# Kernel tuning notes

Measured on AMD Instinct MI355X. Metric: run time of the kernel, lower is better.

The kernel has to match this reference:

```python
import jax, jax.numpy as jnp
import numpy as np

N, C, R, G, K = 4096, 128, 128, 6, 16
RADIUS = 0.8
C_OUT = 64
FLAT = G * G * G * C_OUT  # 13824


def setup_inputs() -> dict:
    key = jax.random.key(0)
    ks = jax.random.split(key, 24)
    xav = lambda k, shp: (jax.random.normal(k, shp, jnp.float32)
                          * np.sqrt(2.0 / (shp[0] + shp[1])).astype(np.float32))
    # scene points in ~[-5,5]^3 so radius-0.8 balls hold ~8 points on average
    xyz = jax.random.normal(ks[0], (N, 3), jnp.float32) * 2.5
    feats = jax.random.normal(ks[1], (N, C), jnp.float32)
    ctr = jax.random.normal(ks[2], (R, 3), jnp.float32) * 2.5
    size = jax.random.uniform(ks[3], (R, 3), jnp.float32) * 3.0 + 1.0
    yaw = jax.random.uniform(ks[4], (R, 1), jnp.float32) * (2.0 * np.pi)
    rois = jnp.concatenate([ctr, size, yaw], -1)  # [R,7] (x,y,z,dx,dy,dz,ry)
    return {
        'xyz': xyz, 'feats': feats, 'rois': rois,
        'w_m1': xav(ks[5], (3 + C, C_OUT)), 'w_m2': xav(ks[6], (C_OUT, C_OUT)),
        'w_s1': xav(ks[7], (FLAT, 1024)), 'w_s2': xav(ks[8], (1024, 512)),
        'w_c1': xav(ks[9], (512, 1024)), 'w_c2': xav(ks[10], (1024, 512)),
        'w_c3': xav(ks[11], (512, 1)), 'b_c3': jnp.zeros((1,), jnp.float32),
        'w_i1': xav(ks[12], (512, 1024)), 'w_i2': xav(ks[13], (1024, 512)),
        'w_i3': xav(ks[14], (512, 1)), 'b_i3': jnp.zeros((1,), jnp.float32),
        'w_r1': xav(ks[15], (512, 1024)), 'w_r2': xav(ks[16], (1024, 512)),
        'w_r3': jax.random.normal(ks[17], (512, 7), jnp.float32) * 0.001,
        'b_r3': jnp.zeros((7,), jnp.float32),
    }


def _grid_points(rois):
    """get_dense_grid_points + rotate_points_along_z + center shift."""
    i = jnp.arange(G)
    gi, gj, gk = jnp.meshgrid(i, i, i, indexing='ij')
    dense = jnp.stack([gi, gj, gk], -1).reshape(-1, 3).astype(rois.dtype)  # [G^3,3]
    size = rois[:, 3:6]
    local = (dense[None] + 0.5) / G * size[:, None] - size[:, None] * 0.5  # [R,G^3,3]
    c, s = jnp.cos(rois[:, 6])[:, None], jnp.sin(rois[:, 6])[:, None]
    x, y, z = local[..., 0], local[..., 1], local[..., 2]
    rot = jnp.stack([x * c - y * s, x * s + y * c, z], -1)
    return rot + rois[:, None, 0:3]  # [R,G^3,3]


def reference(xyz, feats, rois, w_m1, w_m2, w_s1, w_s2,
              w_c1, w_c2, w_c3, b_c3, w_i1, w_i2, w_i3, b_i3,
              w_r1, w_r2, w_r3, b_r3):
    gp = _grid_points(rois).reshape(-1, 3)  # [M,3], M = R*G^3
    M = gp.shape[0]
    # ball query: first K point indices within RADIUS of each grid point
    d2 = jnp.sum((gp[:, None, :] - xyz[None, :, :]) ** 2, -1)  # [M,N]
    cand = jnp.where(d2 < RADIUS * RADIUS, jnp.arange(N), N)  # invalid -> N
    neg_top, _ = jax.lax.top_k(-cand, K)
    idx = -neg_top  # K smallest candidate indices, ascending-ish
    valid = idx < N
    first = idx[:, :1]
    idx = jnp.where(valid, idx, first)  # pad with first hit (pointnet2 semantics)
    empty = ~valid[:, 0]  # balls with zero neighbors
    idx = jnp.where(empty[:, None], 0, idx)
    # group: relative xyz + point features
    rel = xyz[idx] - gp[:, None, :]               # [M,K,3]
    g = jnp.concatenate([rel, feats[idx]], -1)    # [M,K,3+C]
    # shared per-point MLP (Conv2d 1x1 + identity-init BN + ReLU)
    h = jax.nn.relu(g @ w_m1)
    h = jax.nn.relu(h @ w_m2)                     # [M,K,C_OUT]
    pooled = jnp.max(h, axis=1)                   # max_pool over neighbors
    pooled = jnp.where(empty[:, None], 0.0, pooled)
    flat = pooled.reshape(rois.shape[0], -1)      # [R, G^3*C_OUT]
    # shared FC (Conv1d k=1 stacks) then cls / iou / reg heads
    sfc = jax.nn.relu(jax.nn.relu(flat @ w_s1) @ w_s2)
    head = lambda x, w1, w2, w3, b3: jax.nn.relu(jax.nn.relu(x @ w1) @ w2) @ w3 + b3
    cls = head(sfc, w_c1, w_c2, w_c3, b_c3)   # [R,1]
    iou = head(sfc, w_i1, w_i2, w_i3, b_i3)   # [R,1]
    reg = head(sfc, w_r1, w_r2, w_r3, b_r3)   # [R,7]
    return jnp.concatenate([cls, iou, reg], -1)  # [R,9]
```

## Files before the change

kernel.cpp:

```cpp
#include <hip/hip_runtime.h>

typedef float  f32x4  __attribute__((ext_vector_type(4)));
typedef __bf16 bf16x8 __attribute__((ext_vector_type(8)));
typedef unsigned short ushort_t;

#define N_PTS 4096
#define R_ROIS 128
#define M_GP  27648
#define LDS_FENCE() asm volatile("s_waitcnt lgkmcnt(0)" ::: "memory")

static constexpr size_t OFF_GP     = 0;
static constexpr size_t OFF_PH     = 331776;
static constexpr size_t OFF_PL     = 3870720;
static constexpr size_t OFF_H1H    = 331776;
static constexpr size_t OFF_H1L    = 1118208;
static constexpr size_t OFF_H2S    = 1904640;
static constexpr size_t OFF_PART   = 7409664;
static constexpr size_t OFF_CAND   = OFF_PART;
static constexpr size_t OFF_F      = 9506816;
static constexpr size_t OFF_XYZ4   = 10555392;
static constexpr size_t OFF_NCAND  = 11603968;
static constexpr size_t OFF_W1TH   = 11604480;
static constexpr size_t OFF_W1TL   = 11625984;
static constexpr size_t OFF_W2TH   = 11647488;
static constexpr size_t OFF_W2TL   = 11656704;
static constexpr size_t OFF_FHI    = 11665920;
static constexpr size_t OFF_FLO    = 12714496;
static constexpr size_t OFF_IDX    = 11665920;
static constexpr size_t OFF_T1H    = 11665920;
static constexpr size_t OFF_T1L    = 11928064;
static constexpr size_t OFF_SFCH   = 12190208;
static constexpr size_t OFF_SFCL   = 12321280;

static __device__ inline ushort_t f2bf(float f) {
    unsigned int u = __float_as_uint(f);
    unsigned int r = u + 0x7FFFu + ((u >> 16) & 1u);
    return (ushort_t)(r >> 16);
}
static __device__ inline float bf2f(ushort_t h) {
    return __uint_as_float(((unsigned int)h) << 16);
}
static __device__ inline ushort_t bfbits(__bf16 h) {
    return __builtin_bit_cast(ushort_t, h);
}

__global__ __launch_bounds__(256) void prep_all_k(
    const float* __restrict__ rois, const float* __restrict__ xyz,
    const float* __restrict__ feats, const float* __restrict__ w1,
    const float* __restrict__ w2, float* __restrict__ gp,
    ushort_t* __restrict__ fhi, ushort_t* __restrict__ flo,
    ushort_t* __restrict__ w1th, ushort_t* __restrict__ w1tl,
    ushort_t* __restrict__ w2th, ushort_t* __restrict__ w2tl,
    float4* __restrict__ xyz4,
    int* __restrict__ cand, int* __restrict__ ncand) {
    int b = blockIdx.x, tid = threadIdx.x;
    if (b < 108) {
        int m = b * 256 + tid;
        int r = m / 216, t = m % 216;
        int gi = t / 36, gj = (t / 6) % 6, gk = t % 6;
        const float* roi = rois + r * 7;
        float sx = roi[3], sy = roi[4], sz = roi[5];
        float lx = ((float)gi + 0.5f) / 6.0f * sx - sx * 0.5f;
        float ly = ((float)gj + 0.5f) / 6.0f * sy - sy * 0.5f;
        float lz = ((float)gk + 0.5f) / 6.0f * sz - sz * 0.5f;
        float c = cosf(roi[6]), s = sinf(roi[6]);
        gp[m * 3 + 0] = lx * c - ly * s + roi[0];
        gp[m * 3 + 1] = lx * s + ly * c + roi[1];
        gp[m * 3 + 2] = lz + roi[2];
    } else if (b < 150) {
        int t = (b - 108) * 256 + tid;
        {
            int col = t / 168, p = t % 168;
            float v = (p < 128) ? w1[(3 + p) * 64 + col]
                    : (p < 131) ? w1[(p - 128) * 64 + col] : 0.f;
            ushort_t hi = f2bf(v);
            w1th[t] = hi;
            w1tl[t] = f2bf(v - bf2f(hi));
        }
        if (t < 4608) {
            int col = t / 72, k = t % 72;
            float v = (k < 64) ? w2[k * 64 + col] : 0.f;
            ushort_t hi = f2bf(v);
            w2th[t] = hi;
            w2tl[t] = f2bf(v - bf2f(hi));
        }
    } else if (b < 2198) {
        int i = (b - 150) * 256 + tid;
        float v = feats[i];
        __bf16 h = (__bf16)v;
        fhi[i] = bfbits(h);
        flo[i] = bfbits((__bf16)(v - (float)h));
    } else if (b < 2214) {
        int i = (b - 2198) * 256 + tid;
        xyz4[i] = make_float4(xyz[i * 3 + 0], xyz[i * 3 + 1], xyz[i * 3 + 2], 0.f);
    } else {
        int r = (b - 2214) * 4 + (tid >> 6);
        int lane = tid & 63;
        const float* roi = rois + r * 7;
        float cx = roi[0], cy = roi[1], cz = roi[2];
        float sx = roi[3], sy = roi[4], sz = roi[5];
        float Rc = 0.8f + 0.4166667f * sqrtf(sx * sx + sy * sy + sz * sz) + 0.01f;
        float Rc2 = Rc * Rc;
        int* cl = cand + (size_t)r * N_PTS;
        int cnt = 0;
        for (int base = 0; base < N_PTS; base += 64) {
            int i = base + lane;
            float dx = xyz[i * 3 + 0] - cx;
            float dy = xyz[i * 3 + 1] - cy;
            float dz = xyz[i * 3 + 2] - cz;
            bool in = dx * dx + dy * dy + dz * dz < Rc2;
            unsigned long long ball = __ballot(in);
            int before = __popcll(ball & ((1ull << lane) - 1ull));
            if (in) cl[cnt + before] = i;
            cnt += __popcll(ball);
        }
        if (lane == 0) ncand[r] = cnt;
    }
}

__global__ __launch_bounds__(256) void f_gemm_k(
    const ushort_t* __restrict__ fhi, const ushort_t* __restrict__ flo,
    const ushort_t* __restrict__ w1th, const ushort_t* __restrict__ w1tl,
    float* __restrict__ F) {
    int tid = threadIdx.x;
    int w = tid >> 6, lane = tid & 63;
    int row = lane & 15, grp = lane >> 4;
    int m0 = blockIdx.x * 64 + w * 16;

    f32x4 acc[4];
#pragma unroll
    for (int nt = 0; nt < 4; nt++) acc[nt] = {0.f, 0.f, 0.f, 0.f};

#pragma unroll
    for (int ks = 0; ks < 4; ks++) {
        size_t ao = (size_t)(m0 + row) * 128 + ks * 32 + grp * 8;
        bf16x8 ah = *(const bf16x8*)&fhi[ao];
        bf16x8 al = *(const bf16x8*)&flo[ao];
#pragma unroll
        for (int nt = 0; nt < 4; nt++) {
            int bo = (nt * 16 + row) * 168 + ks * 32 + grp * 8;
            bf16x8 bh = *(const bf16x8*)&w1th[bo];
            bf16x8 bl = *(const bf16x8*)&w1tl[bo];
            acc[nt] = __builtin_amdgcn_mfma_f32_16x16x32_bf16(ah, bh, acc[nt], 0, 0, 0);
            acc[nt] = __builtin_amdgcn_mfma_f32_16x16x32_bf16(al, bh, acc[nt], 0, 0, 0);
            acc[nt] = __builtin_amdgcn_mfma_f32_16x16x32_bf16(ah, bl, acc[nt], 0, 0, 0);
        }
    }
#pragma unroll
    for (int nt = 0; nt < 4; nt++)
#pragma unroll
        for (int reg = 0; reg < 4; reg++)
            F[(size_t)(m0 + grp * 4 + reg) * 64 + nt * 16 + row] = acc[nt][reg];
}

__global__ __launch_bounds__(256) void scan_k(
    const float4* __restrict__ xyz4, const float* __restrict__ gp,
    const int* __restrict__ cand, const int* __restrict__ ncand,
    int* __restrict__ idxout) {
    __shared__ int s_idx[4][4][16];
    int tid = threadIdx.x;
    int w = tid >> 6, lane = tid & 63;
    const float R2 = (float)(0.8 * 0.8);
    int m0 = (blockIdx.x * 4 + w) * 4;
    int r = m0 / 216;

    float gxv[4], gyv[4], gzv[4];
#pragma unroll
    for (int g = 0; g < 4; g++) {
        int m = m0 + g;
        gxv[g] = gp[m * 3 + 0];
        gyv[g] = gp[m * 3 + 1];
        gzv[g] = gp[m * 3 + 2];
    }

    int nc = ncand[r];
    const int* cl = cand + (size_t)r * N_PTS;
    int cnt0 = 0, cnt1 = 0, cnt2 = 0, cnt3 = 0;
    for (int base = 0; base < nc; base += 64) {
        int t = base + lane;
        float px = 1e30f, py = 1e30f, pz = 1e30f;
        int i = 0;
        if (t < nc) {
            i = cl[t];
            float4 p = xyz4[i];
            px = p.x; py = p.y; pz = p.z;
        }
#pragma unroll
        for (int g = 0; g < 4; g++) {
            float dx = px - gxv[g], dy = py - gyv[g], dz = pz - gzv[g];
            bool in = dx * dx + dy * dy + dz * dz < R2;
            unsigned long long ball = __ballot(in);
            int before = __popcll(ball & ((1ull << lane) - 1ull));
            int cnt = (g == 0) ? cnt0 : (g == 1) ? cnt1 : (g == 2) ? cnt2 : cnt3;
            int pos = cnt + before;
            if (in && pos < 16) s_idx[w][g][pos] = i;
            int add = __popcll(ball);
            if (g == 0) cnt0 += add; else if (g == 1) cnt1 += add;
            else if (g == 2) cnt2 += add; else cnt3 += add;
        }
        if (cnt0 >= 16 && cnt1 >= 16 && cnt2 >= 16 && cnt3 >= 16) break;
    }
    LDS_FENCE();

#pragma unroll
    for (int g = 0; g < 4; g++) {
        int cnt = (g == 0) ? cnt0 : (g == 1) ? cnt1 : (g == 2) ? cnt2 : cnt3;
        int c = min(cnt, 16);
        if (lane < 16) {
            int v;
            if (c == 0) {
                v = -1;
            } else {
                int f = s_idx[w][g][0];
                v = (lane < c) ? s_idx[w][g][lane] : f;
            }
            idxout[(size_t)(m0 + g) * 16 + lane] = v;
        }
    }
}

__global__ __launch_bounds__(256) void mlp_k(
    const float4* __restrict__ xyz4, const float* __restrict__ F,
    const float* __restrict__ gp, const int* __restrict__ idx,
    const float* __restrict__ w_m1,
    const ushort_t* __restrict__ w2th, const ushort_t* __restrict__ w2tl,
    ushort_t* __restrict__ Afh, ushort_t* __restrict__ Afl) {
    int tid = threadIdx.x;
    int w = tid >> 6, lane = tid & 63;
    int row = lane & 15, grp = lane >> 4;
    int m0 = (blockIdx.x * 4 + w) * 4;
    int r = m0 / 216;

    int pi[4];
    bool empty[4];
    float rx[4], ry[4], rz[4];
#pragma unroll
    for (int g = 0; g < 4; g++) {
        int m = m0 + g;
        int iv = idx[(size_t)m * 16 + row];
        empty[g] = (iv < 0);
        pi[g] = empty[g] ? 0 : iv;
        float4 p = xyz4[pi[g]];
        rx[g] = p.x - gp[m * 3 + 0];
        ry[g] = p.y - gp[m * 3 + 1];
        rz[g] = p.z - gp[m * 3 + 2];
    }

    f32x4 p[4][4];
#pragma unroll
    for (int g = 0; g < 4; g++)
#pragma unroll
        for (int nt = 0; nt < 4; nt++) p[g][nt] = {0.f, 0.f, 0.f, 0.f};

#pragma unroll
    for (int ks = 0; ks < 2; ks++) {
        float w1r0[8], w1r1[8], w1r2[8];
        {
            const float* wp = w_m1 + ks * 32 + grp * 8;
            *(float4*)&w1r0[0] = *(const float4*)(wp);
            *(float4*)&w1r0[4] = *(const float4*)(wp + 4);
            *(float4*)&w1r1[0] = *(const float4*)(wp + 64);
            *(float4*)&w1r1[4] = *(const float4*)(wp + 68);
            *(float4*)&w1r2[0] = *(const float4*)(wp + 128);
            *(float4*)&w1r2[4] = *(const float4*)(wp + 132);
        }
        bf16x8 zah[4], zal[4];
#pragma unroll
        for (int g = 0; g < 4; g++) {
            const float* Fr = F + (size_t)pi[g] * 64 + ks * 32 + grp * 8;
            float fv[8];
            *(float4*)&fv[0] = *(const float4*)Fr;
            *(float4*)&fv[4] = *(const float4*)(Fr + 4);
            bf16x8 hh, ll;
#pragma unroll
            for (int j = 0; j < 8; j++) {
                float zv = fv[j] + rx[g] * w1r0[j] + ry[g] * w1r1[j] + rz[g] * w1r2[j];
                float v = fmaxf(zv, 0.f);
                __bf16 h = (__bf16)v;
                hh[j] = h;
                ll[j] = (__bf16)(v - (float)h);
            }
            zah[g] = hh; zal[g] = ll;
        }
#pragma unroll
        for (int nt = 0; nt < 4; nt++) {
            int bo = (nt * 16 + row) * 72 + ks * 32 + grp * 8;
            bf16x8 bh = *(const bf16x8*)&w2th[bo];
            bf16x8 bl = *(const bf16x8*)&w2tl[bo];
#pragma unroll
            for (int g = 0; g < 4; g++) {
                p[g][nt] = __builtin_amdgcn_mfma_f32_16x16x32_bf16(zah[g], bh, p[g][nt], 0, 0, 0);
                p[g][nt] = __builtin_amdgcn_mfma_f32_16x16x32_bf16(zal[g], bh, p[g][nt], 0, 0, 0);
                p[g][nt] = __builtin_amdgcn_mfma_f32_16x16x32_bf16(zah[g], bl, p[g][nt], 0, 0, 0);
            }
        }
    }

#pragma unroll
    for (int g = 0; g < 4; g++) {
        int m = m0 + g;
        int t = m % 216;
#pragma unroll
        for (int nt = 0; nt < 4; nt++) {
            float mv = fmaxf(fmaxf(fmaxf(p[g][nt][0], p[g][nt][1]),
                                   fmaxf(p[g][nt][2], p[g][nt][3])), 0.f);
            mv = fmaxf(mv, __shfl_xor(mv, 16));
            mv = fmaxf(mv, __shfl_xor(mv, 32));
            if (grp == 0) {
                float v = empty[g] ? 0.f : mv;
                __bf16 h = (__bf16)v;
                int kt = t * 2 + (nt >> 1);
                size_t o = ((size_t)kt * 128 + r) * 32 + (nt & 1) * 16 + row;
                Afh[o] = bfbits(h);
                Afl[o] = bfbits((__bf16)(v - (float)h));
            }
        }
    }
}

__global__ __launch_bounds__(256) void gemm_stream_k(
    const ushort_t* __restrict__ A_h, const ushort_t* __restrict__ A_l,
    size_t a_stride,
    const float* __restrict__ B0, const float* __restrict__ B1,
    const float* __restrict__ B2,
    float* __restrict__ P, int N, int Kt, int S) {
    __shared__ __attribute__((aligned(16))) ushort_t Bs_h[32][40];
    __shared__ __attribute__((aligned(16))) ushort_t Bs_l[32][40];
    int tid = threadIdx.x;
    int w = tid >> 6, lane = tid & 63;
    int row = lane & 15, grp = lane >> 4;
    int z = blockIdx.z, head = z / S, s = z % S;
    int n0 = blockIdx.x * 32, m0 = blockIdx.y * 64;
    const float* B = (head == 0) ? B0 : (head == 1) ? B1 : B2;
    const ushort_t* Ah = A_h + (size_t)head * a_stride;
    const ushort_t* Al = A_l + (size_t)head * a_stride;
    const int STEPS = Kt / (32 * S);
    int kt0 = s * STEPS;
    int nl = tid & 31, kg = tid >> 5;

    f32x4 acc0 = {0.f, 0.f, 0.f, 0.f};
    f32x4 acc1 = {0.f, 0.f, 0.f, 0.f};
    int arow = m0 + w * 16 + row;
    const float* bbase = B + ((size_t)kt0 * 32 + kg * 4) * N + n0 + nl;
    size_t abase = ((size_t)kt0 * 128 + arow) * 32 + grp * 8;

#define LOADB(t, dst)                                                         \
    do {                                                                      \
        const float* bp_ = bbase + (size_t)(t) * 32 * N;                      \
        dst.x = bp_[0];                                                       \
        dst.y = bp_[(size_t)N];                                               \
        dst.z = bp_[(size_t)2 * N];                                           \
        dst.w = bp_[(size_t)3 * N];                                           \
    } while (0)
#define LOADA(t, dh, dl)                                                      \
    do {                                                                      \
        size_t ao_ = abase + (size_t)(t) * 4096;                              \
        dh = *(const bf16x8*)&Ah[ao_];                                        \
        dl = *(const bf16x8*)&Al[ao_];                                        \
    } while (0)
#define STAGE(bv)                                                             \
    do {                                                                      \
        ushort_t hs0 = f2bf(bv.x), ls0;                                       \
        ls0 = f2bf(bv.x - bf2f(hs0));                                         \
        ushort_t hs1 = f2bf(bv.y), ls1;                                       \
        ls1 = f2bf(bv.y - bf2f(hs1));                                         \
        ushort_t hs2 = f2bf(bv.z), ls2;                                       \
        ls2 = f2bf(bv.z - bf2f(hs2));                                         \
        ushort_t hs3 = f2bf(bv.w), ls3;                                       \
        ls3 = f2bf(bv.w - bf2f(hs3));                                         \
        uint2 hw_ = make_uint2((unsigned)hs0 | ((unsigned)hs1 << 16),         \
                               (unsigned)hs2 | ((unsigned)hs3 << 16));        \
        uint2 lw_ = make_uint2((unsigned)ls0 | ((unsigned)ls1 << 16),         \
                               (unsigned)ls2 | ((unsigned)ls3 << 16));        \
        *(uint2*)&Bs_h[nl][kg * 4] = hw_;                                     \
        *(uint2*)&Bs_l[nl][kg * 4] = lw_;                                     \
    } while (0)
#define COMPUTE(ah_, al_)                                                     \
    do {                                                                      \
        bf16x8 bh0 = *(const bf16x8*)&Bs_h[row][grp * 8];                     \
        bf16x8 bl0 = *(const bf16x8*)&Bs_l[row][grp * 8];                     \
        acc0 = __builtin_amdgcn_mfma_f32_16x16x32_bf16(ah_, bh0, acc0, 0, 0, 0); \
        acc0 = __builtin_amdgcn_mfma_f32_16x16x32_bf16(al_, bh0, acc0, 0, 0, 0); \
        acc0 = __builtin_amdgcn_mfma_f32_16x16x32_bf16(ah_, bl0, acc0, 0, 0, 0); \
        bf16x8 bh1 = *(const bf16x8*)&Bs_h[16 + row][grp * 8];                \
        bf16x8 bl1 = *(const bf16x8*)&Bs_l[16 + row][grp * 8];                \
        acc1 = __builtin_amdgcn_mfma_f32_16x16x32_bf16(ah_, bh1, acc1, 0, 0, 0); \
        acc1 = __builtin_amdgcn_mfma_f32_16x16x32_bf16(al_, bh1, acc1, 0, 0, 0); \
        acc1 = __builtin_amdgcn_mfma_f32_16x16x32_bf16(ah_, bl1, acc1, 0, 0, 0); \
    } while (0)

    float4 bv0, bv1;
    bf16x8 a0h, a0l, a1h, a1l;
    LOADB(0, bv0);
    LOADA(0, a0h, a0l);
    LOADB(1, bv1);
    LOADA(1, a1h, a1l);

    for (int t = 0; t < STEPS; t += 2) {
        STAGE(bv0);
        __syncthreads();
        COMPUTE(a0h, a0l);
        if (t + 2 < STEPS) {
            LOADB(t + 2, bv0);
            LOADA(t + 2, a0h, a0l);
        }
        __syncthreads();
        STAGE(bv1);
        __syncthreads();
        COMPUTE(a1h, a1l);
        if (t + 3 < STEPS) {
            LOADB(t + 3, bv1);
            LOADA(t + 3, a1h, a1l);
        }
        __syncthreads();
    }
#undef LOADB
#undef LOADA
#undef STAGE
#undef COMPUTE

    size_t pb = (size_t)z * 128 * N;
#pragma unroll
    for (int reg = 0; reg < 4; reg++) {
        int mrow = m0 + w * 16 + grp * 4 + reg;
        P[pb + (size_t)mrow * N + n0 + row] = acc0[reg];
        P[pb + (size_t)mrow * N + n0 + 16 + row] = acc1[reg];
    }
}

__global__ __launch_bounds__(256) void reduce_frag_k(
    const float* __restrict__ P, ushort_t* __restrict__ C_h,
    ushort_t* __restrict__ C_l, float* __restrict__ C_f, int out_f32,
    int MNper, int S, int heads, int Nn) {
    int i = blockIdx.x * 256 + threadIdx.x;
    if (i >= heads * MNper) return;
    int h = i / MNper, j = i % MNper;
    float v = 0.f;
    for (int s = 0; s < S; s++) v += P[((size_t)(h * S + s)) * MNper + j];
    v = fmaxf(v, 0.f);
    if (out_f32) {
        C_f[i] = v;
        return;
    }
    int m = j / Nn, n = j % Nn;
    size_t off = (size_t)h * MNper + ((size_t)(n >> 5) * 128 + m) * 32 + (n & 31);
    __bf16 hh = (__bf16)v;
    C_h[off] = bfbits(hh);
    C_l[off] = bfbits((__bf16)(v - (float)hh));
}

__global__ __launch_bounds__(256) void head_out3_k(
    const float* __restrict__ h2s, const float* __restrict__ w_c3,
    const float* __restrict__ w_i3, const float* __restrict__ w_r3,
    const float* __restrict__ b_c3, const float* __restrict__ b_i3,
    const float* __restrict__ b_r3, float* __restrict__ out) {
    int t = blockIdx.x * 256 + threadIdx.x;
    if (t >= 128 * 9) return;
    int r = t / 9, col = t % 9;
    int head = (col == 0) ? 0 : (col == 1) ? 1 : 2;
    int p = (col < 2) ? 0 : col - 2;
    int Pn = (head == 2) ? 7 : 1;
    const float* h2 = h2s + (size_t)head * (128 * 512) + (size_t)r * 512;
    const float* w3 = (head == 0) ? w_c3 : (head == 1) ? w_i3 : w_r3;
    float acc = ((head == 0) ? b_c3 : (head == 1) ? b_i3 : b_r3)[p];
    for (int j = 0; j < 512; j++) acc += h2[j] * w3[j * Pn + p];
    out[r * 9 + col] = acc;
}

extern "C" void kernel_launch(void* const* d_in, const int* in_sizes, int n_in,
                              void* d_out, int out_size, void* d_ws, size_t ws_size,
                              hipStream_t stream) {
    const float* xyz   = (const float*)d_in[0];
    const float* feats = (const float*)d_in[1];
    const float* rois  = (const float*)d_in[2];
    const float* w_m1  = (const float*)d_in[3];
    const float* w_m2  = (const float*)d_in[4];
    const float* w_s1  = (const float*)d_in[5];
    const float* w_s2  = (const float*)d_in[6];
    const float* w_c1  = (const float*)d_in[7];
    const float* w_c2  = (const float*)d_in[8];
    const float* w_c3  = (const float*)d_in[9];
    const float* b_c3  = (const float*)d_in[10];
    const float* w_i1  = (const float*)d_in[11];
    const float* w_i2  = (const float*)d_in[12];
    const float* w_i3  = (const float*)d_in[13];
    const float* b_i3  = (const float*)d_in[14];
    const float* w_r1  = (const float*)d_in[15];
    const float* w_r2  = (const float*)d_in[16];
    const float* w_r3  = (const float*)d_in[17];
    const float* b_r3  = (const float*)d_in[18];
    float* out = (float*)d_out;

    char* ws = (char*)d_ws;
    float*    gp     = (float*)(ws + OFF_GP);
    ushort_t* afh    = (ushort_t*)(ws + OFF_PH);
    ushort_t* afl    = (ushort_t*)(ws + OFF_PL);
    float*    part   = (float*)(ws + OFF_PART);
    int*      cand   = (int*)(ws + OFF_CAND);
    float*    F      = (float*)(ws + OFF_F);
    float4*   xyz4   = (float4*)(ws + OFF_XYZ4);
    int*      ncand  = (int*)(ws + OFF_NCAND);
    ushort_t* w1th   = (ushort_t*)(ws + OFF_W1TH);
    ushort_t* w1tl   = (ushort_t*)(ws + OFF_W1TL);
    ushort_t* w2th   = (ushort_t*)(ws + OFF_W2TH);
    ushort_t* w2tl   = (ushort_t*)(ws + OFF_W2TL);
    ushort_t* fhi    = (ushort_t*)(ws + OFF_FHI);
    ushort_t* flo    = (ushort_t*)(ws + OFF_FLO);
    int*      idx    = (int*)(ws + OFF_IDX);
    ushort_t* t1h    = (ushort_t*)(ws + OFF_T1H);
    ushort_t* t1l    = (ushort_t*)(ws + OFF_T1L);
    ushort_t* sfch   = (ushort_t*)(ws + OFF_SFCH);
    ushort_t* sfcl   = (ushort_t*)(ws + OFF_SFCL);
    ushort_t* h1h    = (ushort_t*)(ws + OFF_H1H);
    ushort_t* h1l    = (ushort_t*)(ws + OFF_H1L);
    float*    h2s    = (float*)(ws + OFF_H2S);

    hipLaunchKernelGGL(prep_all_k, dim3(2246), dim3(256), 0, stream,
                       rois, xyz, feats, w_m1, w_m2, gp, fhi, flo,
                       w1th, w1tl, w2th, w2tl, xyz4, cand, ncand);
    hipLaunchKernelGGL(f_gemm_k, dim3(64), dim3(256), 0, stream,
                       fhi, flo, w1th, w1tl, F);
    hipLaunchKernelGGL(scan_k, dim3(M_GP / 16), dim3(256), 0, stream,
                       xyz4, gp, cand, ncand, idx);
    hipLaunchKernelGGL(mlp_k, dim3(M_GP / 16), dim3(256), 0, stream,
                       xyz4, F, gp, idx, w_m1, w2th, w2tl, afh, afl);
    hipLaunchKernelGGL(gemm_stream_k, dim3(32, 2, 8), dim3(256), 0, stream,
                       afh, afl, (size_t)0, w_s1, w_s1, w_s1, part, 1024, 13824, 8);
    hipLaunchKernelGGL(reduce_frag_k, dim3(512), dim3(256), 0, stream,
                       part, t1h, t1l, (float*)nullptr, 0, 128 * 1024, 8, 1, 1024);
    hipLaunchKernelGGL(gemm_stream_k, dim3(16, 2, 8), dim3(256), 0, stream,
                       t1h, t1l, (size_t)0, w_s2, w_s2, w_s2, part, 512, 1024, 8);
    hipLaunchKernelGGL(reduce_frag_k, dim3(256), dim3(256), 0, stream,
                       part, sfch, sfcl, (float*)nullptr, 0, 128 * 512, 8, 1, 512);
    hipLaunchKernelGGL(gemm_stream_k, dim3(32, 2, 6), dim3(256), 0, stream,
                       sfch, sfcl, (size_t)0, w_c1, w_i1, w_r1, part, 1024, 512, 2);
    hipLaunchKernelGGL(reduce_frag_k, dim3(1536), dim3(256), 0, stream,
                       part, h1h, h1l, (float*)nullptr, 0, 128 * 1024, 2, 3, 1024);
    hipLaunchKernelGGL(gemm_stream_k, dim3(16, 2, 12), dim3(256), 0, stream,
                       h1h, h1l, (size_t)131072, w_c2, w_i2, w_r2, part, 512, 1024, 4);
    hipLaunchKernelGGL(reduce_frag_k, dim3(768), dim3(256), 0, stream,
                       part, (ushort_t*)nullptr, (ushort_t*)nullptr, h2s, 1,
                       128 * 512, 4, 3, 512);
    hipLaunchKernelGGL(head_out3_k, dim3(5), dim3(256), 0, stream,
                       h2s, w_c3, w_i3, w_r3, b_c3, b_i3, b_r3, out);
}
```

Baseline: 169.1 us.

## Load B fragments directly into registers, dropping LDS staging and barriers

The streamed split-K GEMM no longer stages the fp32 weight tile through shared memory with bf16 hi/lo conversion and four barriers per step pair. Instead, each lane loads the 16 fp32 B values it needs straight from global memory, splits them into hi/lo bf16 in registers and feeds the MFMAs. This removes LDS traffic and synchronisation. In exchange, B conversion work is duplicated across the 4 waves, there are 4x more global B loads per block (served by cache), and register pressure rises from holding 32 prefetched floats.

```diff
diff --git a/kernel.cpp b/kernel.cpp
--- a/kernel.cpp
+++ b/kernel.cpp
@@ -318,14 +318,12 @@
     }
 }
 
-__global__ __launch_bounds__(256) void gemm_stream_k(
+__global__ __launch_bounds__(256) void gemm_direct_k(
     const ushort_t* __restrict__ A_h, const ushort_t* __restrict__ A_l,
     size_t a_stride,
     const float* __restrict__ B0, const float* __restrict__ B1,
     const float* __restrict__ B2,
     float* __restrict__ P, int N, int Kt, int S) {
-    __shared__ __attribute__((aligned(16))) ushort_t Bs_h[32][40];
-    __shared__ __attribute__((aligned(16))) ushort_t Bs_l[32][40];
     int tid = threadIdx.x;
     int w = tid >> 6, lane = tid & 63;
     int row = lane & 15, grp = lane >> 4;
@@ -336,21 +334,25 @@
     const ushort_t* Al = A_l + (size_t)head * a_stride;
     const int STEPS = Kt / (32 * S);
     int kt0 = s * STEPS;
-    int nl = tid & 31, kg = tid >> 5;
 
     f32x4 acc0 = {0.f, 0.f, 0.f, 0.f};
     f32x4 acc1 = {0.f, 0.f, 0.f, 0.f};
     int arow = m0 + w * 16 + row;
-    const float* bbase = B + ((size_t)kt0 * 32 + kg * 4) * N + n0 + nl;
     size_t abase = ((size_t)kt0 * 128 + arow) * 32 + grp * 8;
-
-#define LOADB(t, dst)                                                         \
+    const float* bbase = B + ((size_t)kt0 * 32 + grp * 8) * (size_t)N + n0 + row;
+    size_t Ns = (size_t)N;
+
+#define DECLB(v) float v##00, v##01, v##02, v##03, v##04, v##05, v##06, v##07, \
+                       v##10, v##11, v##12, v##13, v##14, v##15, v##16, v##17
+#define LOADB(t, v)                                                           \
     do {                                                                      \
-        const float* bp_ = bbase + (size_t)(t) * 32 * N;                      \
-        dst.x = bp_[0];                                                       \
-        dst.y = bp_[(size_t)N];                                               \
-        dst.z = bp_[(size_t)2 * N];                                           \
-        dst.w = bp_[(size_t)3 * N];                                           \
+        const float* p_ = bbase + (size_t)(t) * 32 * Ns;                      \
+        v##00 = p_[0];       v##01 = p_[Ns];      v##02 = p_[2 * Ns];         \
+        v##03 = p_[3 * Ns];  v##04 = p_[4 * Ns];  v##05 = p_[5 * Ns];         \
+        v##06 = p_[6 * Ns];  v##07 = p_[7 * Ns];                              \
+        v##10 = p_[16];          v##11 = p_[Ns + 16];     v##12 = p_[2 * Ns + 16]; \
+        v##13 = p_[3 * Ns + 16]; v##14 = p_[4 * Ns + 16]; v##15 = p_[5 * Ns + 16]; \
+        v##16 = p_[6 * Ns + 16]; v##17 = p_[7 * Ns + 16];                     \
     } while (0)
 #define LOADA(t, dh, dl)                                                      \
     do {                                                                      \
@@ -358,66 +360,52 @@
         dh = *(const bf16x8*)&Ah[ao_];                                        \
         dl = *(const bf16x8*)&Al[ao_];                                        \
     } while (0)
-#define STAGE(bv)                                                             \
+#define C1(x, vh, vl, i)                                                      \
+    { __bf16 hh_ = (__bf16)(x); vh[i] = hh_; vl[i] = (__bf16)((x) - (float)hh_); }
+#define STEPI(v, ah_, al_)                                                    \
     do {                                                                      \
-        ushort_t hs0 = f2bf(bv.x), ls0;                                       \
-        ls0 = f2bf(bv.x - bf2f(hs0));                                         \
-        ushort_t hs1 = f2bf(bv.y), ls1;                                       \
-        ls1 = f2bf(bv.y - bf2f(hs1));                                         \
-        ushort_t hs2 = f2bf(bv.z), ls2;                                       \
-        ls2 = f2bf(bv.z - bf2f(hs2));                                         \
-        ushort_t hs3 = f2bf(bv.w), ls3;                                       \
-        ls3 = f2bf(bv.w - bf2f(hs3));                                         \
-        uint2 hw_ = make_uint2((unsigned)hs0 | ((unsigned)hs1 << 16),         \
-                               (unsigned)hs2 | ((unsigned)hs3 << 16));        \
-        uint2 lw_ = make_uint2((unsigned)ls0 | ((unsigned)ls1 << 16),         \
-                               (unsigned)ls2 | ((unsigned)ls3 << 16));        \
-        *(uint2*)&Bs_h[nl][kg * 4] = hw_;                                     \
-        *(uint2*)&Bs_l[nl][kg * 4] = lw_;                                     \
+        bf16x8 bh0_, bl0_, bh1_, bl1_;                                        \
+        C1(v##00, bh0_, bl0_, 0) C1(v##01, bh0_, bl0_, 1)                     \
+        C1(v##02, bh0_, bl0_, 2) C1(v##03, bh0_, bl0_, 3)                     \
+        C1(v##04, bh0_, bl0_, 4) C1(v##05, bh0_, bl0_, 5)                     \
+        C1(v##06, bh0_, bl0_, 6) C1(v##07, bh0_, bl0_, 7)                     \
+        C1(v##10, bh1_, bl1_, 0) C1(v##11, bh1_, bl1_, 1)                     \
+        C1(v##12, bh1_, bl1_, 2) C1(v##13, bh1_, bl1_, 3)                     \
+        C1(v##14, bh1_, bl1_, 4) C1(v##15, bh1_, bl1_, 5)                     \
+        C1(v##16, bh1_, bl1_, 6) C1(v##17, bh1_, bl1_, 7)                     \
+        acc0 = __builtin_amdgcn_mfma_f32_16x16x32_bf16(ah_, bh0_, acc0, 0, 0, 0); \
+        acc0 = __builtin_amdgcn_mfma_f32_16x16x32_bf16(al_, bh0_, acc0, 0, 0, 0); \
+        acc0 = __builtin_amdgcn_mfma_f32_16x16x32_bf16(ah_, bl0_, acc0, 0, 0, 0); \
+        acc1 = __builtin_amdgcn_mfma_f32_16x16x32_bf16(ah_, bh1_, acc1, 0, 0, 0); \
+        acc1 = __builtin_amdgcn_mfma_f32_16x16x32_bf16(al_, bh1_, acc1, 0, 0, 0); \
+        acc1 = __builtin_amdgcn_mfma_f32_16x16x32_bf16(ah_, bl1_, acc1, 0, 0, 0); \
     } while (0)
-#define COMPUTE(ah_, al_)                                                     \
-    do {                                                                      \
-        bf16x8 bh0 = *(const bf16x8*)&Bs_h[row][grp * 8];                     \
-        bf16x8 bl0 = *(const bf16x8*)&Bs_l[row][grp * 8];                     \
-        acc0 = __builtin_amdgcn_mfma_f32_16x16x32_bf16(ah_, bh0, acc0, 0, 0, 0); \
-        acc0 = __builtin_amdgcn_mfma_f32_16x16x32_bf16(al_, bh0, acc0, 0, 0, 0); \
-        acc0 = __builtin_amdgcn_mfma_f32_16x16x32_bf16(ah_, bl0, acc0, 0, 0, 0); \
-        bf16x8 bh1 = *(const bf16x8*)&Bs_h[16 + row][grp * 8];                \
-        bf16x8 bl1 = *(const bf16x8*)&Bs_l[16 + row][grp * 8];                \
-        acc1 = __builtin_amdgcn_mfma_f32_16x16x32_bf16(ah_, bh1, acc1, 0, 0, 0); \
-        acc1 = __builtin_amdgcn_mfma_f32_16x16x32_bf16(al_, bh1, acc1, 0, 0, 0); \
-        acc1 = __builtin_amdgcn_mfma_f32_16x16x32_bf16(ah_, bl1, acc1, 0, 0, 0); \
-    } while (0)
-
-    float4 bv0, bv1;
+
+    DECLB(q0);
+    DECLB(q1);
     bf16x8 a0h, a0l, a1h, a1l;
-    LOADB(0, bv0);
+    LOADB(0, q0);
     LOADA(0, a0h, a0l);
-    LOADB(1, bv1);
+    LOADB(1, q1);
     LOADA(1, a1h, a1l);
 
     for (int t = 0; t < STEPS; t += 2) {
-        STAGE(bv0);
-        __syncthreads();
-        COMPUTE(a0h, a0l);
+        STEPI(q0, a0h, a0l);
         if (t + 2 < STEPS) {
-            LOADB(t + 2, bv0);
+            LOADB(t + 2, q0);
             LOADA(t + 2, a0h, a0l);
         }
-        __syncthreads();
-        STAGE(bv1);
-        __syncthreads();
-        COMPUTE(a1h, a1l);
+        STEPI(q1, a1h, a1l);
         if (t + 3 < STEPS) {
-            LOADB(t + 3, bv1);
+            LOADB(t + 3, q1);
             LOADA(t + 3, a1h, a1l);
         }
-        __syncthreads();
-    }
+    }
+#undef DECLB
 #undef LOADB
 #undef LOADA
-#undef STAGE
-#undef COMPUTE
+#undef C1
+#undef STEPI
 
     size_t pb = (size_t)z * 128 * N;
 #pragma unroll
@@ -524,19 +512,19 @@
                        xyz4, gp, cand, ncand, idx);
     hipLaunchKernelGGL(mlp_k, dim3(M_GP / 16), dim3(256), 0, stream,
                        xyz4, F, gp, idx, w_m1, w2th, w2tl, afh, afl);
-    hipLaunchKernelGGL(gemm_stream_k, dim3(32, 2, 8), dim3(256), 0, stream,
+    hipLaunchKernelGGL(gemm_direct_k, dim3(32, 2, 8), dim3(256), 0, stream,
                        afh, afl, (size_t)0, w_s1, w_s1, w_s1, part, 1024, 13824, 8);
     hipLaunchKernelGGL(reduce_frag_k, dim3(512), dim3(256), 0, stream,
                        part, t1h, t1l, (float*)nullptr, 0, 128 * 1024, 8, 1, 1024);
-    hipLaunchKernelGGL(gemm_stream_k, dim3(16, 2, 8), dim3(256), 0, stream,
+    hipLaunchKernelGGL(gemm_direct_k, dim3(16, 2, 8), dim3(256), 0, stream,
                        t1h, t1l, (size_t)0, w_s2, w_s2, w_s2, part, 512, 1024, 8);
     hipLaunchKernelGGL(reduce_frag_k, dim3(256), dim3(256), 0, stream,
                        part, sfch, sfcl, (float*)nullptr, 0, 128 * 512, 8, 1, 512);
-    hipLaunchKernelGGL(gemm_stream_k, dim3(32, 2, 6), dim3(256), 0, stream,
+    hipLaunchKernelGGL(gemm_direct_k, dim3(32, 2, 6), dim3(256), 0, stream,
                        sfch, sfcl, (size_t)0, w_c1, w_i1, w_r1, part, 1024, 512, 2);
     hipLaunchKernelGGL(reduce_frag_k, dim3(1536), dim3(256), 0, stream,
                        part, h1h, h1l, (float*)nullptr, 0, 128 * 1024, 2, 3, 1024);
-    hipLaunchKernelGGL(gemm_stream_k, dim3(16, 2, 12), dim3(256), 0, stream,
+    hipLaunchKernelGGL(gemm_direct_k, dim3(16, 2, 12), dim3(256), 0, stream,
                        h1h, h1l, (size_t)131072, w_c2, w_i2, w_r2, part, 512, 1024, 4);
     hipLaunchKernelGGL(reduce_frag_k, dim3(768), dim3(256), 0, stream,
                        part, (ushort_t*)nullptr, (ushort_t*)nullptr, h2s, 1,
```

Result: slower. 173.8 us (+2.8%).
